# Kernel optimization log

Measured on AMD Instinct MI355X. Metric: run time of the kernel, lower is better.

Reference implementation:

```python
import jax, jax.numpy as jnp
import numpy as np

_B, _Q, _D, _H, _L, _F, _C, _HM = 8, 100, 256, 8, 9, 2048, 151, 112


def setup_inputs():
    key = jax.random.key(0)
    ks = list(jax.random.split(key, 40)); ki = [0]
    def nk():
        k = ks[ki[0]]; ki[0] += 1; return k
    def r(shape, s=1.0):
        return jax.random.normal(nk(), shape, jnp.float32) * s
    z, o = jnp.zeros, jnp.ones
    return {
        'mask_features': r((_B, _D, _HM, _HM)),
        'mem0': r((_B, _D, 14, 14)), 'mem1': r((_B, _D, 28, 28)), 'mem2': r((_B, _D, 56, 56)),
        'query_feat': r((_Q, _D), 0.02), 'query_embed': r((_Q, _D), 0.02),
        'ca_wqkv': r((_L, 3, _D, _D), 0.02), 'ca_bqkv': z((_L, 3, _D)),
        'ca_wo': r((_L, _D, _D), 0.02), 'ca_bo': z((_L, _D)),
        'ca_ln_s': o((_L, _D)), 'ca_ln_b': z((_L, _D)),
        'sa_wqkv': r((_L, 3, _D, _D), 0.02), 'sa_bqkv': z((_L, 3, _D)),
        'sa_wo': r((_L, _D, _D), 0.02), 'sa_bo': z((_L, _D)),
        'sa_ln_s': o((_L, _D)), 'sa_ln_b': z((_L, _D)),
        'ffn_w1': r((_L, _D, _F), 0.02), 'ffn_b1': z((_L, _F)),
        'ffn_w2': r((_L, _F, _D), 0.02), 'ffn_b2': z((_L, _D)),
        'ffn_ln_s': o((_L, _D)), 'ffn_ln_b': z((_L, _D)),
        'dec_ln_s': o((_D,)), 'dec_ln_b': z((_D,)),
        'me_w1': r((_D, _D), 0.02), 'me_b1': z((_D,)),
        'me_w2': r((_D, _D), 0.02), 'me_b2': z((_D,)),
        'me_w3': r((_D, _D), 0.02), 'me_b3': z((_D,)),
        'cls_w': r((_D, _C), 0.02), 'cls_b': z((_C,)),
    }


def _ln(x, s, b, eps=1e-5):
    m = x.mean(-1, keepdims=True)
    v = ((x - m) ** 2).mean(-1, keepdims=True)
    return (x - m) * jax.lax.rsqrt(v + eps) * s + b


def _mha(q, k, v, wqkv, bqkv, wo, bo, bias):
    # q: [B,Nq,D]; k,v: [B,Nk,D]; bias: [B,1,Nq,Nk] additive (-1e9 = masked) or None
    B, Nq, D = q.shape
    hd = D // _H
    qh = (q @ wqkv[0] + bqkv[0]).reshape(B, Nq, _H, hd)
    kh = (k @ wqkv[1] + bqkv[1]).reshape(B, -1, _H, hd)
    vh = (v @ wqkv[2] + bqkv[2]).reshape(B, -1, _H, hd)
    scores = jnp.einsum('bqhd,bkhd->bhqk', qh, kh) / np.sqrt(hd).astype(np.float32)
    if bias is not None:
        scores = scores + bias
    attn = jax.nn.softmax(scores, axis=-1)
    out = jnp.einsum('bhqk,bkhd->bqhd', attn, vh).reshape(B, Nq, D)
    return out @ wo + bo


def _attn_bias(prev_mask, hw):
    # prev_mask: [B,Q,Hm,Wm] raw logits -> additive bias [B,1,Q,H*W]
    B, Q = prev_mask.shape[:2]
    r = jax.image.resize(prev_mask, (B, Q) + hw, 'bilinear')  # align_corners=False
    ignore = (jax.nn.sigmoid(r) < 0.5).reshape(B, Q, -1)      # True = masked out
    fully = jnp.all(ignore, axis=-1, keepdims=True)           # un-mask fully-masked rows
    ignore = jnp.where(fully, False, ignore)
    return jnp.where(ignore, jnp.float32(-1e9), jnp.float32(0.0))[:, None]


def _forward(mask_features, mem0, mem1, mem2, query_feat, query_embed,
             ca_wqkv, ca_bqkv, ca_wo, ca_bo, ca_ln_s, ca_ln_b,
             sa_wqkv, sa_bqkv, sa_wo, sa_bo, sa_ln_s, sa_ln_b,
             ffn_w1, ffn_b1, ffn_w2, ffn_b2, ffn_ln_s, ffn_ln_b,
             dec_ln_s, dec_ln_b, me_w1, me_b1, me_w2, me_b2, me_w3, me_b3,
             cls_w, cls_b):
    B, D, Hm, Wm = mask_features.shape
    Q = query_feat.shape[0]
    mems = [(m.reshape(B, D, -1).transpose(0, 2, 1), m.shape[2:]) for m in (mem0, mem1, mem2)]
    mask_flat = mask_features.reshape(B, D, -1).transpose(0, 2, 1)  # [B,Hm*Wm,D]
    q = jnp.broadcast_to((query_feat + query_embed)[None], (B, Q, D))
    prev = None
    for i in range(_L):
        mem, hw = mems[i % 3]
        bias = _attn_bias(prev, hw) if prev is not None else None
        q = _ln(q + _mha(q, mem, mem, ca_wqkv[i], ca_bqkv[i], ca_wo[i], ca_bo[i], bias), ca_ln_s[i], ca_ln_b[i])
        q = _ln(q + _mha(q, q, q, sa_wqkv[i], sa_bqkv[i], sa_wo[i], sa_bo[i], None), sa_ln_s[i], sa_ln_b[i])
        h = jax.nn.relu(q @ ffn_w1[i] + ffn_b1[i]) @ ffn_w2[i] + ffn_b2[i]
        q = _ln(q + h, ffn_ln_s[i], ffn_ln_b[i])
        nq = _ln(q, dec_ln_s, dec_ln_b)
        me = jax.nn.relu(jax.nn.relu(nq @ me_w1 + me_b1) @ me_w2 + me_b2) @ me_w3 + me_b3
        pred_mask = jnp.einsum('bqd,bpd->bqp', me, mask_flat).reshape(B, Q, Hm, Wm)
        prev = jax.lax.stop_gradient(pred_mask)
    pred_logits = nq @ cls_w + cls_b
    return pred_logits, pred_mask


def reference(mask_features, mem0, mem1, mem2, query_feat, query_embed,
              ca_wqkv, ca_bqkv, ca_wo, ca_bo, ca_ln_s, ca_ln_b,
              sa_wqkv, sa_bqkv, sa_wo, sa_bo, sa_ln_s, sa_ln_b,
              ffn_w1, ffn_b1, ffn_w2, ffn_b2, ffn_ln_s, ffn_ln_b,
              dec_ln_s, dec_ln_b, me_w1, me_b1, me_w2, me_b2, me_w3, me_b3,
              cls_w, cls_b):
    return _forward(mask_features, mem0, mem1, mem2, query_feat, query_embed,
                    ca_wqkv, ca_bqkv, ca_wo, ca_bo, ca_ln_s, ca_ln_b,
                    sa_wqkv, sa_bqkv, sa_wo, sa_bo, sa_ln_s, sa_ln_b,
                    ffn_w1, ffn_b1, ffn_w2, ffn_b2, ffn_ln_s, ffn_ln_b,
                    dec_ln_s, dec_ln_b, me_w1, me_b1, me_w2, me_b2, me_w3, me_b3,
                    cls_w, cls_b)
```

## Files before the change

kernel.cpp:

```cpp
#include <hip/hip_runtime.h>
#include <cmath>

#define B_ 8
#define Q_ 100
#define D_ 256
#define H_ 8
#define HD_ 32
#define L_ 9
#define F_ 2048
#define C_ 151
#define HM_ 112
#define PMAX_ 3136
#define KT_ 128
#define RECSZ 544

typedef __attribute__((ext_vector_type(4))) short s4v;
typedef __attribute__((ext_vector_type(8))) short s8v;
typedef __attribute__((ext_vector_type(4))) float f4v;

__device__ __forceinline__ unsigned short f2bf(float x) {
  unsigned int u = __float_as_uint(x);
  return (unsigned short)((u + 0x7fffu + ((u >> 16) & 1u)) >> 16);
}
__device__ __forceinline__ float bf2f(unsigned short h) {
  return __uint_as_float(((unsigned int)h) << 16);
}
__device__ __forceinline__ void split2(float x, short& h, short& l) {
  unsigned short hb = f2bf(x);
  float r = x - bf2f(hb);
  h = (short)hb;
  l = (short)f2bf(r);
}

__device__ __forceinline__ float block_sum(float v, float* red) {
  int t = threadIdx.x;
  red[t] = v; __syncthreads();
  for (int s = 128; s > 0; s >>= 1) {
    if (t < s) red[t] += red[t + s];
    __syncthreads();
  }
  float r = red[0]; __syncthreads();
  return r;
}

__global__ __launch_bounds__(256) void initq_kernel(const float* __restrict__ qf,
                                                    const float* __restrict__ qe,
                                                    float* __restrict__ q) {
  int idx = blockIdx.x * 256 + threadIdx.x;
  int qd = idx % (Q_ * D_);
  q[idx] = qf[qd] + qe[qd];
}

__global__ __launch_bounds__(256) void tsplit_kernel(
    const float* __restrict__ in, short* __restrict__ out,
    int K, int N, long long ibs, long long obs) {
  __shared__ float tile[32][33];
  const int z = blockIdx.z;
  const int nb = blockIdx.x * 32, kb = blockIdx.y * 32;
  const float* I = in + (size_t)z * ibs;
  short* O = out + (size_t)z * obs;
  const int t = threadIdx.x;
  {
    const int r = t >> 3, c = (t & 7) * 4;
    const int gk = kb + r;
#pragma unroll
    for (int j = 0; j < 4; ++j) {
      int gn = nb + c + j;
      tile[r][c + j] = (gk < K && gn < N) ? I[(size_t)gk * N + gn] : 0.f;
    }
  }
  __syncthreads();
  {
    const int nr = t >> 3, kc = (t & 7) * 4;
    const int gn = nb + nr;
    if (gn < N) {
#pragma unroll
      for (int j = 0; j < 4; ++j) {
        int gk = kb + kc + j;
        if (gk < K) {
          short h, l; split2(tile[kc + j][nr], h, l);
          O[(size_t)gn * 2 * K + gk] = h;
          O[(size_t)gn * 2 * K + K + gk] = l;
        }
      }
    }
  }
}

__device__ __forceinline__ s8v ldfrag(const short* p) {
  s4v lo = *(const s4v*)p;
  s4v hi = *(const s4v*)(p + 16);
  return __builtin_shufflevector(lo, hi, 0, 1, 2, 3, 4, 5, 6, 7);
}

template <int BM, int AMODE, int WMODE, bool RELU, int OUT>
__global__ __launch_bounds__(256) void mgemm_kernel(
    const void* __restrict__ Ap, const void* __restrict__ Wp,
    const float* __restrict__ bias, void* __restrict__ Cv,
    int M, int N, int K,
    long long Abs, long long Wbs, long long Cbs, int ldc) {
  constexpr int MI = BM / 32;
  __shared__ short Ah[BM * 36], Al[BM * 36], Wh[128 * 36], Wl[128 * 36];
  const int z = blockIdx.z;
  const int n0 = blockIdx.x * 128, m0 = blockIdx.y * BM;
  const int t = threadIdx.x;
  const int lane = t & 63;
  const int wave = t >> 6;
  const int wm = wave >> 1, wn = wave & 1;
  const int lr = lane & 15, lg = lane >> 4;
  f4v acc[MI][4];
#pragma unroll
  for (int i = 0; i < MI; ++i)
#pragma unroll
    for (int j = 0; j < 4; ++j) acc[i][j] = (f4v){0.f, 0.f, 0.f, 0.f};

  for (int k0 = 0; k0 < K; k0 += 32) {
    if (AMODE == 0) {
      const float* A = (const float*)Ap + (size_t)z * Abs;
      if (BM == 64) {
        const int arow = t >> 2;
        const int kc = (t & 3) * 8;
        float x[8];
        if (m0 + arow < M) {
          const float* ap = A + (size_t)(m0 + arow) * K + k0 + kc;
          *(f4v*)&x[0] = *(const f4v*)ap;
          *(f4v*)&x[4] = *(const f4v*)(ap + 4);
        } else {
#pragma unroll
          for (int e = 0; e < 8; ++e) x[e] = 0.f;
        }
        s4v h0, h1, l0, l1;
#pragma unroll
        for (int e = 0; e < 4; ++e) { short hh, ll; split2(x[e], hh, ll); h0[e] = hh; l0[e] = ll; }
#pragma unroll
        for (int e = 0; e < 4; ++e) { short hh, ll; split2(x[4 + e], hh, ll); h1[e] = hh; l1[e] = ll; }
        *(s4v*)&Ah[arow * 36 + kc] = h0; *(s4v*)&Ah[arow * 36 + kc + 4] = h1;
        *(s4v*)&Al[arow * 36 + kc] = l0; *(s4v*)&Al[arow * 36 + kc + 4] = l1;
      } else {
        const int arow = t >> 3;
        const int kc = (t & 7) * 4;
        float x[4];
        if (m0 + arow < M) {
          *(f4v*)&x[0] = *(const f4v*)(A + (size_t)(m0 + arow) * K + k0 + kc);
        } else {
#pragma unroll
          for (int e = 0; e < 4; ++e) x[e] = 0.f;
        }
        s4v h0, l0;
#pragma unroll
        for (int e = 0; e < 4; ++e) { short hh, ll; split2(x[e], hh, ll); h0[e] = hh; l0[e] = ll; }
        *(s4v*)&Ah[arow * 36 + kc] = h0;
        *(s4v*)&Al[arow * 36 + kc] = l0;
      }
    } else {
      const short* A2 = (const short*)Ap + (size_t)z * Abs;
      const int arow = t >> 2;
      const int c = t & 3, sel = c >> 1, ko = (c & 1) * 16;
      s8v v0 = {0, 0, 0, 0, 0, 0, 0, 0}, v1 = {0, 0, 0, 0, 0, 0, 0, 0};
      if (m0 + arow < M) {
        const short* ap = A2 + (size_t)(m0 + arow) * (2 * K) + sel * K + k0 + ko;
        v0 = *(const s8v*)ap;
        v1 = *(const s8v*)(ap + 8);
      }
      short* dst = sel ? Al : Ah;
      *(s4v*)&dst[arow * 36 + ko] = __builtin_shufflevector(v0, v0, 0, 1, 2, 3);
      *(s4v*)&dst[arow * 36 + ko + 4] = __builtin_shufflevector(v0, v0, 4, 5, 6, 7);
      *(s4v*)&dst[arow * 36 + ko + 8] = __builtin_shufflevector(v1, v1, 0, 1, 2, 3);
      *(s4v*)&dst[arow * 36 + ko + 12] = __builtin_shufflevector(v1, v1, 4, 5, 6, 7);
    }
    if (WMODE == 0) {
      const short* W2 = (const short*)Wp + (size_t)z * Wbs;
      const int n = t >> 1, sel = t & 1;
      const short* wp = W2 + (size_t)(n0 + n) * (2 * K) + sel * K + k0;
      short* dst = sel ? Wl : Wh;
#pragma unroll
      for (int j = 0; j < 4; ++j) {
        s8v v = *(const s8v*)(wp + j * 8);
        *(s4v*)&dst[n * 36 + j * 8] = __builtin_shufflevector(v, v, 0, 1, 2, 3);
        *(s4v*)&dst[n * 36 + j * 8 + 4] = __builtin_shufflevector(v, v, 4, 5, 6, 7);
      }
    } else {
      const float* W = (const float*)Wp + (size_t)z * Wbs;
      const int kr = t >> 3, c0 = (t & 7) * 16;
      const float* wp = W + (size_t)(k0 + kr) * N + n0 + c0;
      float x[16];
#pragma unroll
      for (int j = 0; j < 4; ++j) *(f4v*)&x[j * 4] = *(const f4v*)(wp + j * 4);
#pragma unroll
      for (int j = 0; j < 16; ++j) {
        short hh, ll; split2(x[j], hh, ll);
        Wh[(c0 + j) * 36 + kr] = hh;
        Wl[(c0 + j) * 36 + kr] = ll;
      }
    }
    __syncthreads();
    s8v whf[4], wlf[4];
#pragma unroll
    for (int ni = 0; ni < 4; ++ni) {
      whf[ni] = ldfrag(&Wh[(wn * 64 + ni * 16 + lr) * 36 + 4 * lg]);
      wlf[ni] = ldfrag(&Wl[(wn * 64 + ni * 16 + lr) * 36 + 4 * lg]);
    }
#pragma unroll
    for (int mi = 0; mi < MI; ++mi) {
      s8v ah = ldfrag(&Ah[(wm * (BM / 2) + mi * 16 + lr) * 36 + 4 * lg]);
      s8v al = ldfrag(&Al[(wm * (BM / 2) + mi * 16 + lr) * 36 + 4 * lg]);
#pragma unroll
      for (int ni = 0; ni < 4; ++ni) {
        acc[mi][ni] = __builtin_amdgcn_mfma_f32_16x16x32_bf16(ah, whf[ni], acc[mi][ni], 0, 0, 0);
        acc[mi][ni] = __builtin_amdgcn_mfma_f32_16x16x32_bf16(al, whf[ni], acc[mi][ni], 0, 0, 0);
        acc[mi][ni] = __builtin_amdgcn_mfma_f32_16x16x32_bf16(ah, wlf[ni], acc[mi][ni], 0, 0, 0);
      }
    }
    __syncthreads();
  }
  float* Cf = (float*)Cv + (size_t)z * Cbs;
  unsigned short* Ch = (unsigned short*)Cv + (size_t)z * Cbs;
#pragma unroll
  for (int mi = 0; mi < MI; ++mi) {
#pragma unroll
    for (int i = 0; i < 4; ++i) {
      int row = m0 + wm * (BM / 2) + mi * 16 + 4 * lg + i;
      if (row >= M) continue;
#pragma unroll
      for (int ni = 0; ni < 4; ++ni) {
        int col = n0 + wn * 64 + ni * 16 + lr;
        float v = acc[mi][ni][i] + (bias ? bias[col] : 0.f);
        if (RELU) v = fmaxf(v, 0.f);
        if (OUT == 0) Cf[(size_t)row * ldc + col] = v;
        else Ch[(size_t)row * ldc + col] = f2bf(v);
      }
    }
  }
}

__global__ __launch_bounds__(256) void gemm32_kernel(
    const float* __restrict__ A, const float* __restrict__ W,
    const float* __restrict__ bias, float* __restrict__ C,
    int M, int N, int K) {
  __shared__ float As[16][65];
  __shared__ float Ws[16][65];
  const int n0 = blockIdx.x * 64, m0 = blockIdx.y * 64;
  const int t = threadIdx.x;
  const int tm = t >> 4, tn = t & 15;
  float acc[4][4] = {};
  for (int k0 = 0; k0 < K; k0 += 16) {
#pragma unroll
    for (int l = 0; l < 4; ++l) {
      int idx = t + l * 256;
      int am = idx >> 4, ak = idx & 15;
      int gm = m0 + am, gk = k0 + ak;
      As[ak][am] = (gm < M) ? A[(size_t)gm * K + gk] : 0.f;
      int wk = idx >> 6, wn = idx & 63;
      int gn = n0 + wn, gk2 = k0 + wk;
      Ws[wk][wn] = (gn < N) ? W[(size_t)gk2 * N + gn] : 0.f;
    }
    __syncthreads();
#pragma unroll
    for (int kk = 0; kk < 16; ++kk) {
      float a[4], b[4];
#pragma unroll
      for (int i = 0; i < 4; ++i) a[i] = As[kk][tm * 4 + i];
#pragma unroll
      for (int j = 0; j < 4; ++j) b[j] = Ws[kk][tn * 4 + j];
#pragma unroll
      for (int i = 0; i < 4; ++i)
#pragma unroll
        for (int j = 0; j < 4; ++j) acc[i][j] += a[i] * b[j];
    }
    __syncthreads();
  }
#pragma unroll
  for (int i = 0; i < 4; ++i) {
    int gm = m0 + tm * 4 + i;
    if (gm >= M) continue;
#pragma unroll
    for (int j = 0; j < 4; ++j) {
      int gn = n0 + tn * 4 + j;
      if (gn >= N) continue;
      C[(size_t)gm * N + gn] = acc[i][j] + bias[gn];
    }
  }
}

template <bool RES>
__global__ __launch_bounds__(256) void ln_kernel(const float* __restrict__ x,
                                                 const float* __restrict__ r,
                                                 const float* __restrict__ s,
                                                 const float* __restrict__ b,
                                                 float* __restrict__ out, int nrows) {
  const int wave = threadIdx.x >> 6, lane = threadIdx.x & 63;
  const int row = blockIdx.x * 4 + wave;
  if (row >= nrows) return;
  f4v v = *((const f4v*)(x + (size_t)row * D_) + lane);
  if (RES) {
    f4v rv = *((const f4v*)(r + (size_t)row * D_) + lane);
    v[0] += rv[0]; v[1] += rv[1]; v[2] += rv[2]; v[3] += rv[3];
  }
  float sum = v[0] + v[1] + v[2] + v[3];
#pragma unroll
  for (int off = 32; off > 0; off >>= 1) sum += __shfl_xor(sum, off, 64);
  float mean = sum * (1.f / D_);
  float c0 = v[0] - mean, c1 = v[1] - mean, c2 = v[2] - mean, c3 = v[3] - mean;
  float vs = c0 * c0 + c1 * c1 + c2 * c2 + c3 * c3;
#pragma unroll
  for (int off = 32; off > 0; off >>= 1) vs += __shfl_xor(vs, off, 64);
  float inv = rsqrtf(vs * (1.f / D_) + 1e-5f);
  f4v sv = *((const f4v*)s + lane);
  f4v bv = *((const f4v*)b + lane);
  f4v o;
  o[0] = c0 * inv * sv[0] + bv[0];
  o[1] = c1 * inv * sv[1] + bv[1];
  o[2] = c2 * inv * sv[2] + bv[2];
  o[3] = c3 * inv * sv[3] + bv[3];
  *((f4v*)(out + (size_t)row * D_) + lane) = o;
}

template <bool BIAS, bool KVBF16, bool SPLIT>
__global__ __launch_bounds__(256) void mattn_kernel(
    const float* __restrict__ qb, int ldq,
    const void* __restrict__ kbv, int ldk,
    const void* __restrict__ vbv, int ldv,
    const unsigned int* __restrict__ bits,
    float* __restrict__ outp, int P, int Pw, int tps, int S) {
  __shared__ __align__(16) short Kt[128 * 40];
  __shared__ __align__(16) short Vt[32 * 132];
  __shared__ __align__(16) short Pt[4 * 16 * 36];
  __shared__ unsigned int bb[64];
  __shared__ float Msh[4][16], Lsh[4][16];
  float* Osh = (float*)Kt;
  const int b = blockIdx.x >> 3, h = blockIdx.x & 7;
  const int q0 = blockIdx.y * 16;
  const int seg = blockIdx.z;
  const int kbeg = seg * tps * KT_;
  const int kend = min(P, kbeg + tps * KT_);
  const int t = threadIdx.x;
  const int lane = t & 63, w = t >> 6;
  const int lr = lane & 15, lg = lane >> 4;
  const float scale = 0.17677669529663687f;

  s8v qhf, qlf;
  {
    int qrow = q0 + lr; if (qrow >= Q_) qrow = Q_ - 1;
    const float* qp = qb + (size_t)(b * Q_ + qrow) * ldq + h * HD_;
#pragma unroll
    for (int e = 0; e < 8; ++e) {
      int d = 4 * lg + (e & 3) + 16 * (e >> 2);
      short hh, ll; split2(qp[d], hh, ll);
      qhf[e] = hh; qlf[e] = ll;
    }
  }
  float mreg[4], lreg[4];
  f4v accO0 = (f4v){0.f, 0.f, 0.f, 0.f}, accO1 = (f4v){0.f, 0.f, 0.f, 0.f};
#pragma unroll
  for (int i = 0; i < 4; ++i) { mreg[i] = -3.0e38f; lreg[i] = 0.f; }

  for (int k0 = kbeg; k0 < kend; k0 += KT_) {
    {
      const int key = t >> 1, dh = (t & 1) * 16;
      const int gk = k0 + key;
      s8v ka = {0,0,0,0,0,0,0,0}, kb2 = {0,0,0,0,0,0,0,0};
      s8v va = {0,0,0,0,0,0,0,0}, vb2 = {0,0,0,0,0,0,0,0};
      if (gk < kend) {
        if (KVBF16) {
          const unsigned short* kp = (const unsigned short*)kbv + (size_t)(b * P + gk) * ldk + h * HD_ + dh;
          const unsigned short* vp = (const unsigned short*)vbv + (size_t)(b * P + gk) * ldv + h * HD_ + dh;
          ka = *(const s8v*)kp; kb2 = *(const s8v*)(kp + 8);
          va = *(const s8v*)vp; vb2 = *(const s8v*)(vp + 8);
        } else {
          const float* kp = (const float*)kbv + (size_t)(b * P + gk) * ldk + h * HD_ + dh;
          const float* vp = (const float*)vbv + (size_t)(b * P + gk) * ldv + h * HD_ + dh;
#pragma unroll
          for (int j = 0; j < 8; ++j) {
            ka[j] = (short)f2bf(kp[j]); kb2[j] = (short)f2bf(kp[8 + j]);
            va[j] = (short)f2bf(vp[j]); vb2[j] = (short)f2bf(vp[8 + j]);
          }
        }
      }
      *(s8v*)&Kt[key * 40 + dh] = ka;
      *(s8v*)&Kt[key * 40 + dh + 8] = kb2;
#pragma unroll
      for (int j = 0; j < 8; ++j) {
        Vt[(dh + j) * 132 + key] = va[j];
        Vt[(dh + 8 + j) * 132 + key] = vb2[j];
      }
    }
    if (BIAS && t < 64) {
      int qq = t >> 2, wi = t & 3;
      int gr = q0 + qq, gw = (k0 >> 5) + wi;
      bb[t] = (gr < Q_ && gw < Pw) ? bits[(size_t)(b * Q_ + gr) * Pw + gw] : 0u;
    }
    __syncthreads();
    s8v kf0 = ldfrag(&Kt[(w * 32 + lr) * 40 + 4 * lg]);
    s8v kf1 = ldfrag(&Kt[(w * 32 + 16 + lr) * 40 + 4 * lg]);
    f4v accS0 = (f4v){0.f, 0.f, 0.f, 0.f}, accS1 = (f4v){0.f, 0.f, 0.f, 0.f};
    accS0 = __builtin_amdgcn_mfma_f32_16x16x32_bf16(qhf, kf0, accS0, 0, 0, 0);
    accS0 = __builtin_amdgcn_mfma_f32_16x16x32_bf16(qlf, kf0, accS0, 0, 0, 0);
    accS1 = __builtin_amdgcn_mfma_f32_16x16x32_bf16(qhf, kf1, accS1, 0, 0, 0);
    accS1 = __builtin_amdgcn_mfma_f32_16x16x32_bf16(qlf, kf1, accS1, 0, 0, 0);
    const int gk0 = k0 + w * 32 + lr;
#pragma unroll
    for (int i = 0; i < 4; ++i) {
      float s0 = accS0[i] * scale, s1 = accS1[i] * scale;
      if (BIAS) {
        unsigned int word = bb[(4 * lg + i) * 4 + w];
        if ((word >> lr) & 1u) s0 += -1e9f;
        if ((word >> (16 + lr)) & 1u) s1 += -1e9f;
      }
      if (gk0 >= kend) s0 = -3.0e38f;
      if (gk0 + 16 >= kend) s1 = -3.0e38f;
      float rm = fmaxf(s0, s1);
#pragma unroll
      for (int off = 1; off < 16; off <<= 1) rm = fmaxf(rm, __shfl_xor(rm, off, 64));
      float mn = fmaxf(mreg[i], rm);
      float corr = __expf(mreg[i] - mn);
      mreg[i] = mn;
      float p0 = __expf(s0 - mn), p1 = __expf(s1 - mn);
      lreg[i] = lreg[i] * corr + p0 + p1;
      accO0[i] *= corr;
      accO1[i] *= corr;
      Pt[w * 576 + (4 * lg + i) * 36 + lr] = (short)f2bf(p0);
      Pt[w * 576 + (4 * lg + i) * 36 + 16 + lr] = (short)f2bf(p1);
    }
    s8v pf = ldfrag(&Pt[w * 576 + lr * 36 + 4 * lg]);
    s8v vf0 = ldfrag(&Vt[lr * 132 + w * 32 + 4 * lg]);
    s8v vf1 = ldfrag(&Vt[(16 + lr) * 132 + w * 32 + 4 * lg]);
    accO0 = __builtin_amdgcn_mfma_f32_16x16x32_bf16(pf, vf0, accO0, 0, 0, 0);
    accO1 = __builtin_amdgcn_mfma_f32_16x16x32_bf16(pf, vf1, accO1, 0, 0, 0);
    __syncthreads();
  }
#pragma unroll
  for (int i = 0; i < 4; ++i) {
    float lv = lreg[i];
#pragma unroll
    for (int off = 1; off < 16; off <<= 1) lv += __shfl_xor(lv, off, 64);
    if (lr == 0) { Msh[w][4 * lg + i] = mreg[i]; Lsh[w][4 * lg + i] = lv; }
  }
#pragma unroll
  for (int i = 0; i < 4; ++i) {
    Osh[w * 528 + (4 * lg + i) * 33 + lr] = accO0[i];
    Osh[w * 528 + (4 * lg + i) * 33 + 16 + lr] = accO1[i];
  }
  __syncthreads();
  float* part = SPLIT
      ? outp + ((size_t)((blockIdx.x * gridDim.y + blockIdx.y) * S + seg)) * RECSZ
      : nullptr;
  for (int o = t; o < 512; o += 256) {
    int qq = o >> 5, d = o & 31;
    float M = fmaxf(fmaxf(Msh[0][qq], Msh[1][qq]), fmaxf(Msh[2][qq], Msh[3][qq]));
    float lt = 0.f, Ov = 0.f;
#pragma unroll
    for (int w4 = 0; w4 < 4; ++w4) {
      float wt = __expf(Msh[w4][qq] - M);
      lt += wt * Lsh[w4][qq];
      Ov += wt * Osh[w4 * 528 + qq * 33 + d];
    }
    if (SPLIT) {
      if (d == 0) { part[qq] = M; part[16 + qq] = lt; }
      part[32 + qq * 32 + d] = Ov;
    } else if (q0 + qq < Q_) {
      outp[(size_t)(b * Q_ + q0 + qq) * D_ + h * HD_ + d] = Ov / lt;
    }
  }
}

__global__ __launch_bounds__(256) void attncomb_kernel(
    const float* __restrict__ part, float* __restrict__ out, int S, int nqt) {
  const int row = blockIdx.x;
  const int b = row / Q_, qq = row % Q_;
  const int t = threadIdx.x;
  const int h = t >> 5, d = t & 31;
  const int qt = qq >> 4, r = qq & 15;
  const float* base = part + ((size_t)((b * 8 + h) * nqt + qt) * S) * RECSZ;
  float M = -3.0e38f;
  for (int s = 0; s < S; ++s) M = fmaxf(M, base[(size_t)s * RECSZ + r]);
  float lt = 0.f, Ov = 0.f;
  for (int s = 0; s < S; ++s) {
    const float* rec = base + (size_t)s * RECSZ;
    float w = __expf(rec[r] - M);
    lt += w * rec[16 + r];
    Ov += w * rec[32 + r * 32 + d];
  }
  out[(size_t)row * D_ + h * HD_ + d] = Ov / lt;
}

__global__ __launch_bounds__(256) void maskbias_kernel(
    const float* __restrict__ prev,
    unsigned int* __restrict__ bias,
    int oh) {
  __shared__ float pm[HM_ * HM_];
  __shared__ float rbuf[PMAX_];
  __shared__ float red[256];
  __shared__ unsigned int bw[128];
  const int row = blockIdx.x;
  const int t = threadIdx.x;
  const float* src = prev + (size_t)row * (HM_ * HM_);
  for (int i = t; i < HM_ * HM_; i += 256) pm[i] = src[i];
  __syncthreads();
  const int ratio = HM_ / oh;
  const int taps = 2 * ratio;
  const float invr = 1.f / (float)ratio;
  const int P = oh * oh;
  const int Pw = (P + 31) >> 5;
  float nign = 0.f;
  for (int p = t; p < P; p += 256) {
    int oy = p / oh, ox = p - oy * oh;
    float sy = (oy + 0.5f) * ratio - 0.5f;
    float sx = (ox + 0.5f) * ratio - 0.5f;
    int y0 = (int)floorf(sy - ratio) + 1;
    int x0 = (int)floorf(sx - ratio) + 1;
    float wxs = 0.f;
    for (int si = 0; si < taps; ++si) {
      int x = x0 + si;
      if (x < 0 || x >= HM_) continue;
      wxs += 1.f - fabsf(sx - x) * invr;
    }
    float acc = 0.f, wys = 0.f;
    for (int ti = 0; ti < taps; ++ti) {
      int y = y0 + ti;
      if (y < 0 || y >= HM_) continue;
      float wy = 1.f - fabsf(sy - y) * invr;
      wys += wy;
      float ra = 0.f;
      const float* pr = pm + y * HM_;
      for (int si = 0; si < taps; ++si) {
        int x = x0 + si;
        if (x < 0 || x >= HM_) continue;
        float wx = 1.f - fabsf(sx - x) * invr;
        ra += wx * pr[x];
      }
      acc += wy * ra;
    }
    float rv = acc / (wys * wxs);
    rbuf[p] = rv;
    if (!(rv < 0.f)) nign += 1.f;
  }
  float tot = block_sum(nign, red);
  bool fully = (tot == 0.f);
  for (int w = t; w < Pw; w += 256) bw[w] = 0u;
  __syncthreads();
  if (!fully) {
    for (int p = t; p < P; p += 256) {
      if (rbuf[p] < 0.f) atomicOr(&bw[p >> 5], 1u << (p & 31));
    }
  }
  __syncthreads();
  unsigned int* dst = bias + (size_t)row * Pw;
  for (int w = t; w < Pw; w += 256) dst[w] = bw[w];
}

static inline void mg(hipStream_t st, int bm, int amode, int wmode, bool relu,
                      const void* A, const void* W, const float* bias, void* C,
                      int M, int N, int K, int Z,
                      long long Abs, long long Wbs, long long Cbs, int ldc) {
  dim3 g(N / 128, (M + bm - 1) / bm, Z);
  if (bm == 32) {
    if (relu)
      mgemm_kernel<32, 0, 0, true, 0><<<g, 256, 0, st>>>(A, W, bias, C, M, N, K, Abs, Wbs, Cbs, ldc);
    else
      mgemm_kernel<32, 0, 0, false, 0><<<g, 256, 0, st>>>(A, W, bias, C, M, N, K, Abs, Wbs, Cbs, ldc);
  } else {
    if (amode == 1)
      mgemm_kernel<64, 1, 0, false, 1><<<g, 256, 0, st>>>(A, W, bias, C, M, N, K, Abs, Wbs, Cbs, ldc);
    else if (wmode == 1)
      mgemm_kernel<64, 0, 1, false, 0><<<g, 256, 0, st>>>(A, W, bias, C, M, N, K, Abs, Wbs, Cbs, ldc);
    else
      mgemm_kernel<64, 0, 0, false, 0><<<g, 256, 0, st>>>(A, W, bias, C, M, N, K, Abs, Wbs, Cbs, ldc);
  }
}

extern "C" void kernel_launch(void* const* d_in, const int* in_sizes, int n_in,
                              void* d_out, int out_size, void* d_ws, size_t ws_size,
                              hipStream_t stream) {
  const float* mask_features = (const float*)d_in[0];
  const float* mem[3] = {(const float*)d_in[1], (const float*)d_in[2], (const float*)d_in[3]};
  const float* qf = (const float*)d_in[4];
  const float* qe = (const float*)d_in[5];
  const float* ca_wqkv = (const float*)d_in[6];
  const float* ca_bqkv = (const float*)d_in[7];
  const float* ca_wo = (const float*)d_in[8];
  const float* ca_bo = (const float*)d_in[9];
  const float* ca_ln_s = (const float*)d_in[10];
  const float* ca_ln_b = (const float*)d_in[11];
  const float* sa_wqkv = (const float*)d_in[12];
  const float* sa_bqkv = (const float*)d_in[13];
  const float* sa_wo = (const float*)d_in[14];
  const float* sa_bo = (const float*)d_in[15];
  const float* sa_ln_s = (const float*)d_in[16];
  const float* sa_ln_b = (const float*)d_in[17];
  const float* ffn_w1 = (const float*)d_in[18];
  const float* ffn_b1 = (const float*)d_in[19];
  const float* ffn_w2 = (const float*)d_in[20];
  const float* ffn_b2 = (const float*)d_in[21];
  const float* ffn_ln_s = (const float*)d_in[22];
  const float* ffn_ln_b = (const float*)d_in[23];
  const float* dec_ln_s = (const float*)d_in[24];
  const float* dec_ln_b = (const float*)d_in[25];
  const float* me_w1 = (const float*)d_in[26];
  const float* me_b1 = (const float*)d_in[27];
  const float* me_w2 = (const float*)d_in[28];
  const float* me_b2 = (const float*)d_in[29];
  const float* me_w3 = (const float*)d_in[30];
  const float* me_b3 = (const float*)d_in[31];
  const float* cls_w = (const float*)d_in[32];
  const float* cls_b = (const float*)d_in[33];

  float* out_logits = (float*)d_out;
  float* out_mask = (float*)d_out + (size_t)800 * C_;

  float* fws = (float*)d_ws;
  float* q      = fws; fws += (size_t)800 * D_;
  float* qh     = fws; fws += (size_t)800 * D_;
  float* attn_o = fws; fws += (size_t)800 * D_;
  float* tmp    = fws; fws += (size_t)800 * D_;
  float* nq     = fws; fws += (size_t)800 * D_;
  float* me1    = fws; fws += (size_t)800 * D_;
  float* me2    = fws; fws += (size_t)800 * D_;
  float* me3    = fws; fws += (size_t)800 * D_;
  float* kvbuf  = fws; fws += (size_t)B_ * PMAX_ * 256;
  float* qkvbuf = fws; fws += (size_t)800 * 768;
  float* biasb  = fws; fws += (size_t)800 * 128;
  float* ffnh   = fws; fws += (size_t)B_ * Q_ * F_;
  float* part   = fws; fws += (size_t)64 * 7 * 3 * RECSZ;

  unsigned short* kvb = (unsigned short*)kvbuf;
  unsigned int* biasbits = (unsigned int*)biasb;

  short* sws = (short*)fws;
  short* W2ca  = sws; sws += (size_t)27 * 256 * 512;
  short* W2sa  = sws; sws += (size_t)27 * 256 * 512;
  short* W2cao = sws; sws += (size_t)9 * 256 * 512;
  short* W2sao = sws; sws += (size_t)9 * 256 * 512;
  short* W2f1  = sws; sws += (size_t)9 * 2048 * 512;
  short* W2f2  = sws; sws += (size_t)9 * 256 * 4096;
  short* W2me  = sws; sws += (size_t)3 * 256 * 512;
  short* mem2s = sws; sws += (size_t)B_ * 3136 * 512;
  short* mem1s = sws; sws += (size_t)B_ * 784 * 512;
  short* mem0s = sws; sws += (size_t)B_ * 196 * 512;
  short* memsp[3] = {mem0s, mem1s, mem2s};
  short* maskfs = sws; sws += (size_t)B_ * 12544 * 512;
  const bool presplit = ((size_t)((char*)sws - (char*)d_ws) <= ws_size);

  tsplit_kernel<<<dim3(8, 8, 27), 256, 0, stream>>>(ca_wqkv, W2ca, 256, 256, 65536, 131072);
  tsplit_kernel<<<dim3(8, 8, 27), 256, 0, stream>>>(sa_wqkv, W2sa, 256, 256, 65536, 131072);
  tsplit_kernel<<<dim3(8, 8, 9), 256, 0, stream>>>(ca_wo, W2cao, 256, 256, 65536, 131072);
  tsplit_kernel<<<dim3(8, 8, 9), 256, 0, stream>>>(sa_wo, W2sao, 256, 256, 65536, 131072);
  tsplit_kernel<<<dim3(64, 8, 9), 256, 0, stream>>>(ffn_w1, W2f1, 256, 2048, 524288, 1048576);
  tsplit_kernel<<<dim3(8, 64, 9), 256, 0, stream>>>(ffn_w2, W2f2, 2048, 256, 524288, 1048576);
  tsplit_kernel<<<dim3(8, 8, 1), 256, 0, stream>>>(me_w1, W2me, 256, 256, 0, 0);
  tsplit_kernel<<<dim3(8, 8, 1), 256, 0, stream>>>(me_w2, W2me + 131072, 256, 256, 0, 0);
  tsplit_kernel<<<dim3(8, 8, 1), 256, 0, stream>>>(me_w3, W2me + 262144, 256, 256, 0, 0);
  tsplit_kernel<<<dim3(7, 8, 8), 256, 0, stream>>>(mem[0], mem0s, 256, 196, 256 * 196, 196 * 512);
  tsplit_kernel<<<dim3(25, 8, 8), 256, 0, stream>>>(mem[1], mem1s, 256, 784, 256 * 784, 784 * 512);
  tsplit_kernel<<<dim3(98, 8, 8), 256, 0, stream>>>(mem[2], mem2s, 256, 3136, 256 * 3136, 3136 * 512);
  if (presplit)
    tsplit_kernel<<<dim3(392, 8, 8), 256, 0, stream>>>(mask_features, maskfs, 256, 12544,
                                                       (long long)256 * 12544,
                                                       (long long)12544 * 512);

  initq_kernel<<<800, 256, 0, stream>>>(qf, qe, q);

  const int Ps[3] = {196, 784, 3136};
  const int ohs[3] = {14, 28, 56};
  const int Ss[3] = {1, 2, 3};
  for (int i = 0; i < L_; ++i) {
    const int mi = i % 3, P = Ps[mi], oh = ohs[mi];
    const int Pw = (P + 31) >> 5;
    const int S = Ss[mi];
    const int ntiles = (P + KT_ - 1) / KT_;
    const int tps = (ntiles + S - 1) / S;
    if (i > 0) maskbias_kernel<<<800, 256, 0, stream>>>(out_mask, biasbits, oh);
    mg(stream, 32, 0, 0, false, q, W2ca + (size_t)(i * 3) * 131072, ca_bqkv + i * 768, qh,
       800, 256, 256, 1, 0, 0, 0, 256);
    mg(stream, 64, 1, 0, false, memsp[mi], W2ca + (size_t)(i * 3 + 1) * 131072,
       ca_bqkv + i * 768 + 256, kvb,
       P, 512, 256, B_, (long long)P * 512, 0, (long long)P * 512, 512);
    {
      dim3 ag(64, 7, S);
      if (S > 1) {
        if (i > 0)
          mattn_kernel<true, true, true><<<ag, 256, 0, stream>>>(
              qh, 256, kvb, 512, kvb + 256, 512, biasbits, part, P, Pw, tps, S);
        else
          mattn_kernel<false, true, true><<<ag, 256, 0, stream>>>(
              qh, 256, kvb, 512, kvb + 256, 512, nullptr, part, P, Pw, tps, S);
        attncomb_kernel<<<800, 256, 0, stream>>>(part, attn_o, S, 7);
      } else {
        if (i > 0)
          mattn_kernel<true, true, false><<<ag, 256, 0, stream>>>(
              qh, 256, kvb, 512, kvb + 256, 512, biasbits, attn_o, P, Pw, tps, S);
        else
          mattn_kernel<false, true, false><<<ag, 256, 0, stream>>>(
              qh, 256, kvb, 512, kvb + 256, 512, nullptr, attn_o, P, Pw, tps, S);
      }
    }
    mg(stream, 32, 0, 0, false, attn_o, W2cao + (size_t)i * 131072, ca_bo + i * 256, tmp,
       800, 256, 256, 1, 0, 0, 0, 256);
    ln_kernel<true><<<200, 256, 0, stream>>>(tmp, q, ca_ln_s + i * 256, ca_ln_b + i * 256, q, 800);
    mg(stream, 32, 0, 0, false, q, W2sa + (size_t)(i * 3) * 131072, sa_bqkv + i * 768, qkvbuf,
       800, 768, 256, 1, 0, 0, 0, 768);
    mattn_kernel<false, false, false><<<dim3(64, 7, 1), 256, 0, stream>>>(
        qkvbuf, 768, qkvbuf + 256, 768, qkvbuf + 512, 768, nullptr, attn_o, 100, 4, 1, 1);
    mg(stream, 32, 0, 0, false, attn_o, W2sao + (size_t)i * 131072, sa_bo + i * 256, tmp,
       800, 256, 256, 1, 0, 0, 0, 256);
    ln_kernel<true><<<200, 256, 0, stream>>>(tmp, q, sa_ln_s + i * 256, sa_ln_b + i * 256, q, 800);
    mg(stream, 32, 0, 0, true, q, W2f1 + (size_t)i * 1048576, ffn_b1 + i * 2048, ffnh,
       800, 2048, 256, 1, 0, 0, 0, 2048);
    mg(stream, 32, 0, 0, false, ffnh, W2f2 + (size_t)i * 1048576, ffn_b2 + i * 256, tmp,
       800, 256, 2048, 1, 0, 0, 0, 256);
    ln_kernel<true><<<200, 256, 0, stream>>>(tmp, q, ffn_ln_s + i * 256, ffn_ln_b + i * 256, q, 800);
    ln_kernel<false><<<200, 256, 0, stream>>>(q, nullptr, dec_ln_s, dec_ln_b, nq, 800);
    mg(stream, 32, 0, 0, true, nq, W2me, me_b1, me1, 800, 256, 256, 1, 0, 0, 0, 256);
    mg(stream, 32, 0, 0, true, me1, W2me + 131072, me_b2, me2, 800, 256, 256, 1, 0, 0, 0, 256);
    mg(stream, 32, 0, 0, false, me2, W2me + 262144, me_b3, me3, 800, 256, 256, 1, 0, 0, 0, 256);
    if (presplit)
      mg(stream, 64, 0, 0, false, me3, maskfs, nullptr, out_mask,
         100, 12544, 256, B_, (long long)100 * 256, (long long)12544 * 512,
         (long long)100 * 12544, 12544);
    else
      mg(stream, 64, 0, 1, false, me3, mask_features, nullptr, out_mask,
         100, 12544, 256, B_, (long long)100 * 256, (long long)256 * 12544,
         (long long)100 * 12544, 12544);
  }
  gemm32_kernel<<<dim3(3, 13, 1), 256, 0, stream>>>(nq, cls_w, cls_b, out_logits, 800, C_, 256);
}
```

Baseline: 3.353 ms.

## Fuse decoder LayerNorm and mask-embed MLP into one kernel; drop mask_features presplit

Adds a maskhead kernel that does the decoder LayerNorm and the three 256x256 mask-embed layers in one launch per 16-row tile, keeping intermediates in shared memory instead of four separate launches and global round-trips. The big mask_features bf16 hi/lo presplit pass and its workspace are removed. The mask GEMM now always reads the fp32 mask features directly (WMODE=1) with swapped grid indexing, so the two M-tiles sharing the same mask-feature columns run next to each other. The fused kernel launches only 50 blocks, which limits parallelism. The direct fp32 read may cost more inside the GEMM than the one-time presplit did.

```diff
diff --git a/kernel.cpp b/kernel.cpp
--- a/kernel.cpp
+++ b/kernel.cpp
@@ -98,11 +98,13 @@
     const void* __restrict__ Ap, const void* __restrict__ Wp,
     const float* __restrict__ bias, void* __restrict__ Cv,
     int M, int N, int K,
-    long long Abs, long long Wbs, long long Cbs, int ldc) {
+    long long Abs, long long Wbs, long long Cbs, int ldc, int swap) {
   constexpr int MI = BM / 32;
   __shared__ short Ah[BM * 36], Al[BM * 36], Wh[128 * 36], Wl[128 * 36];
   const int z = blockIdx.z;
-  const int n0 = blockIdx.x * 128, m0 = blockIdx.y * BM;
+  const int bx = swap ? blockIdx.y : blockIdx.x;
+  const int by = swap ? blockIdx.x : blockIdx.y;
+  const int n0 = bx * 128, m0 = by * BM;
   const int t = threadIdx.x;
   const int lane = t & 63;
   const int wave = t >> 6;
@@ -230,6 +232,104 @@
         else Ch[(size_t)row * ldc + col] = f2bf(v);
       }
     }
+  }
+}
+
+__global__ __launch_bounds__(256) void maskhead_kernel(
+    const float* __restrict__ q, const float* __restrict__ lns,
+    const float* __restrict__ lnb, const short* __restrict__ W123,
+    const float* __restrict__ b1, const float* __restrict__ b2,
+    const float* __restrict__ b3,
+    float* __restrict__ nqout, float* __restrict__ me3out) {
+  __shared__ float Xb[16 * 264], Yb[16 * 264];
+  __shared__ short Ah[16 * 36], Al[16 * 36], Wh[256 * 36], Wl[256 * 36];
+  const int r0 = blockIdx.x * 16;
+  const int t = threadIdx.x;
+  const int lane = t & 63, w = t >> 6;
+  const int lr = lane & 15, lg = lane >> 4;
+#pragma unroll
+  for (int rr = 0; rr < 4; ++rr) {
+    int row = w * 4 + rr;
+    int grow = r0 + row;
+    f4v v = *((const f4v*)(q + (size_t)grow * D_) + lane);
+    float sum = v[0] + v[1] + v[2] + v[3];
+#pragma unroll
+    for (int off = 32; off > 0; off >>= 1) sum += __shfl_xor(sum, off, 64);
+    float mean = sum * (1.f / D_);
+    float c0 = v[0] - mean, c1 = v[1] - mean, c2 = v[2] - mean, c3 = v[3] - mean;
+    float vs = c0 * c0 + c1 * c1 + c2 * c2 + c3 * c3;
+#pragma unroll
+    for (int off = 32; off > 0; off >>= 1) vs += __shfl_xor(vs, off, 64);
+    float inv = rsqrtf(vs * (1.f / D_) + 1e-5f);
+    f4v sv = *((const f4v*)lns + lane);
+    f4v bv = *((const f4v*)lnb + lane);
+    f4v o;
+    o[0] = c0 * inv * sv[0] + bv[0];
+    o[1] = c1 * inv * sv[1] + bv[1];
+    o[2] = c2 * inv * sv[2] + bv[2];
+    o[3] = c3 * inv * sv[3] + bv[3];
+    *(f4v*)&Xb[row * 264 + lane * 4] = o;
+    *((f4v*)(nqout + (size_t)grow * D_) + lane) = o;
+  }
+  __syncthreads();
+  float* src = Xb;
+  float* dst = Yb;
+  for (int s = 0; s < 3; ++s) {
+    const short* Ws = W123 + (size_t)s * 131072;
+    const float* bs = (s == 0) ? b1 : ((s == 1) ? b2 : b3);
+    f4v acc[4];
+#pragma unroll
+    for (int j = 0; j < 4; ++j) acc[j] = (f4v){0.f, 0.f, 0.f, 0.f};
+    for (int k0 = 0; k0 < 256; k0 += 32) {
+      {
+        int idx = t * 2;
+        int row = idx >> 5, kc = idx & 31;
+        short h0, l0, h1, l1;
+        split2(src[row * 264 + k0 + kc], h0, l0);
+        split2(src[row * 264 + k0 + kc + 1], h1, l1);
+        Ah[row * 36 + kc] = h0; Ah[row * 36 + kc + 1] = h1;
+        Al[row * 36 + kc] = l0; Al[row * 36 + kc + 1] = l1;
+      }
+      {
+        const short* wp = Ws + (size_t)t * 512 + k0;
+#pragma unroll
+        for (int j = 0; j < 8; ++j)
+          *(s4v*)&Wh[t * 36 + j * 4] = *(const s4v*)(wp + j * 4);
+        const short* wpl = wp + 256;
+#pragma unroll
+        for (int j = 0; j < 8; ++j)
+          *(s4v*)&Wl[t * 36 + j * 4] = *(const s4v*)(wpl + j * 4);
+      }
+      __syncthreads();
+      s8v ah = ldfrag(&Ah[lr * 36 + 4 * lg]);
+      s8v al = ldfrag(&Al[lr * 36 + 4 * lg]);
+#pragma unroll
+      for (int ni = 0; ni < 4; ++ni) {
+        s8v wh = ldfrag(&Wh[(w * 64 + ni * 16 + lr) * 36 + 4 * lg]);
+        s8v wl = ldfrag(&Wl[(w * 64 + ni * 16 + lr) * 36 + 4 * lg]);
+        acc[ni] = __builtin_amdgcn_mfma_f32_16x16x32_bf16(ah, wh, acc[ni], 0, 0, 0);
+        acc[ni] = __builtin_amdgcn_mfma_f32_16x16x32_bf16(al, wh, acc[ni], 0, 0, 0);
+        acc[ni] = __builtin_amdgcn_mfma_f32_16x16x32_bf16(ah, wl, acc[ni], 0, 0, 0);
+      }
+      __syncthreads();
+    }
+#pragma unroll
+    for (int ni = 0; ni < 4; ++ni) {
+#pragma unroll
+      for (int i = 0; i < 4; ++i) {
+        int row = 4 * lg + i;
+        int col = w * 64 + ni * 16 + lr;
+        float v = acc[ni][i] + bs[col];
+        if (s < 2) v = fmaxf(v, 0.f);
+        dst[row * 264 + col] = v;
+      }
+    }
+    __syncthreads();
+    float* tmpp = src; src = dst; dst = tmpp;
+  }
+  for (int o = t; o < 16 * 256; o += 256) {
+    int row = o >> 8, col = o & 255;
+    me3out[(size_t)(r0 + row) * D_ + col] = src[row * 264 + col];
   }
 }
 
@@ -555,16 +655,14 @@
   dim3 g(N / 128, (M + bm - 1) / bm, Z);
   if (bm == 32) {
     if (relu)
-      mgemm_kernel<32, 0, 0, true, 0><<<g, 256, 0, st>>>(A, W, bias, C, M, N, K, Abs, Wbs, Cbs, ldc);
+      mgemm_kernel<32, 0, 0, true, 0><<<g, 256, 0, st>>>(A, W, bias, C, M, N, K, Abs, Wbs, Cbs, ldc, 0);
     else
-      mgemm_kernel<32, 0, 0, false, 0><<<g, 256, 0, st>>>(A, W, bias, C, M, N, K, Abs, Wbs, Cbs, ldc);
+      mgemm_kernel<32, 0, 0, false, 0><<<g, 256, 0, st>>>(A, W, bias, C, M, N, K, Abs, Wbs, Cbs, ldc, 0);
   } else {
     if (amode == 1)
-      mgemm_kernel<64, 1, 0, false, 1><<<g, 256, 0, st>>>(A, W, bias, C, M, N, K, Abs, Wbs, Cbs, ldc);
-    else if (wmode == 1)
-      mgemm_kernel<64, 0, 1, false, 0><<<g, 256, 0, st>>>(A, W, bias, C, M, N, K, Abs, Wbs, Cbs, ldc);
+      mgemm_kernel<64, 1, 0, false, 1><<<g, 256, 0, st>>>(A, W, bias, C, M, N, K, Abs, Wbs, Cbs, ldc, 0);
     else
-      mgemm_kernel<64, 0, 0, false, 0><<<g, 256, 0, st>>>(A, W, bias, C, M, N, K, Abs, Wbs, Cbs, ldc);
+      mgemm_kernel<64, 0, 0, false, 0><<<g, 256, 0, st>>>(A, W, bias, C, M, N, K, Abs, Wbs, Cbs, ldc, 0);
   }
 }
 
@@ -613,8 +711,6 @@
   float* attn_o = fws; fws += (size_t)800 * D_;
   float* tmp    = fws; fws += (size_t)800 * D_;
   float* nq     = fws; fws += (size_t)800 * D_;
-  float* me1    = fws; fws += (size_t)800 * D_;
-  float* me2    = fws; fws += (size_t)800 * D_;
   float* me3    = fws; fws += (size_t)800 * D_;
   float* kvbuf  = fws; fws += (size_t)B_ * PMAX_ * 256;
   float* qkvbuf = fws; fws += (size_t)800 * 768;
@@ -637,8 +733,6 @@
   short* mem1s = sws; sws += (size_t)B_ * 784 * 512;
   short* mem0s = sws; sws += (size_t)B_ * 196 * 512;
   short* memsp[3] = {mem0s, mem1s, mem2s};
-  short* maskfs = sws; sws += (size_t)B_ * 12544 * 512;
-  const bool presplit = ((size_t)((char*)sws - (char*)d_ws) <= ws_size);
 
   tsplit_kernel<<<dim3(8, 8, 27), 256, 0, stream>>>(ca_wqkv, W2ca, 256, 256, 65536, 131072);
   tsplit_kernel<<<dim3(8, 8, 27), 256, 0, stream>>>(sa_wqkv, W2sa, 256, 256, 65536, 131072);
@@ -652,10 +746,6 @@
   tsplit_kernel<<<dim3(7, 8, 8), 256, 0, stream>>>(mem[0], mem0s, 256, 196, 256 * 196, 196 * 512);
   tsplit_kernel<<<dim3(25, 8, 8), 256, 0, stream>>>(mem[1], mem1s, 256, 784, 256 * 784, 784 * 512);
   tsplit_kernel<<<dim3(98, 8, 8), 256, 0, stream>>>(mem[2], mem2s, 256, 3136, 256 * 3136, 3136 * 512);
-  if (presplit)
-    tsplit_kernel<<<dim3(392, 8, 8), 256, 0, stream>>>(mask_features, maskfs, 256, 12544,
-                                                       (long long)256 * 12544,
-                                                       (long long)12544 * 512);
 
   initq_kernel<<<800, 256, 0, stream>>>(qf, qe, q);
 
@@ -708,18 +798,11 @@
     mg(stream, 32, 0, 0, false, ffnh, W2f2 + (size_t)i * 1048576, ffn_b2 + i * 256, tmp,
        800, 256, 2048, 1, 0, 0, 0, 256);
     ln_kernel<true><<<200, 256, 0, stream>>>(tmp, q, ffn_ln_s + i * 256, ffn_ln_b + i * 256, q, 800);
-    ln_kernel<false><<<200, 256, 0, stream>>>(q, nullptr, dec_ln_s, dec_ln_b, nq, 800);
-    mg(stream, 32, 0, 0, true, nq, W2me, me_b1, me1, 800, 256, 256, 1, 0, 0, 0, 256);
-    mg(stream, 32, 0, 0, true, me1, W2me + 131072, me_b2, me2, 800, 256, 256, 1, 0, 0, 0, 256);
-    mg(stream, 32, 0, 0, false, me2, W2me + 262144, me_b3, me3, 800, 256, 256, 1, 0, 0, 0, 256);
-    if (presplit)
-      mg(stream, 64, 0, 0, false, me3, maskfs, nullptr, out_mask,
-         100, 12544, 256, B_, (long long)100 * 256, (long long)12544 * 512,
-         (long long)100 * 12544, 12544);
-    else
-      mg(stream, 64, 0, 1, false, me3, mask_features, nullptr, out_mask,
-         100, 12544, 256, B_, (long long)100 * 256, (long long)256 * 12544,
-         (long long)100 * 12544, 12544);
+    maskhead_kernel<<<50, 256, 0, stream>>>(q, dec_ln_s, dec_ln_b, W2me,
+                                            me_b1, me_b2, me_b3, nq, me3);
+    mgemm_kernel<64, 0, 1, false, 0><<<dim3(2, 98, 8), 256, 0, stream>>>(
+        me3, mask_features, nullptr, out_mask, 100, 12544, 256,
+        (long long)100 * 256, (long long)256 * 12544, (long long)100 * 12544, 12544, 1);
   }
   gemm32_kernel<<<dim3(3, 13, 1), 256, 0, stream>>>(nq, cls_w, cls_b, out_logits, 800, C_, 256);
 }
```

New measurement: 3.382 ms. About the same (+0.9%).
